# Kernel optimization log

Measured on AMD Instinct MI355X. Metric: run time of the kernel, lower is better.

## Reference

```python
import jax, jax.numpy as jnp
import numpy as np

FP4_AMAX = 6.0
FP8_AMAX = 448.0
E2M1_LUT = jnp.array([0.0, 0.5, 1.0, 1.5, 2.0, 3.0, 4.0, 6.0], dtype=jnp.float32)
# (threshold, code) pairs; applied in order, alternating <= and < comparisons
THRESHOLDS = [(5.0, 6), (3.5, 5), (2.5, 4), (1.75, 3), (1.25, 2), (0.75, 1), (0.25, 0)]


def _fp4_code(a):
    # a: abs-values, float32. Round-to-e2m1 magnitude code per the torch threshold table.
    code = jnp.full(a.shape, 7, dtype=jnp.int32)
    for i, (m, c) in enumerate(THRESHOLDS):
        mask = (a <= m) if i % 2 == 0 else (a < m)
        code = jnp.where(mask, c, code)
    return code


def simulate_nvfp4_quantize(w):
    # w: (out, in), in % 16 == 0. Returns fake-quantized weight, same shape/dtype.
    out_f, in_f = w.shape
    wb = w.reshape(out_f, in_f // 16, 16).astype(jnp.float32)
    gs = (FP4_AMAX * FP8_AMAX) / jnp.max(jnp.abs(wb))          # global fp32 scale
    s_decb = jnp.max(jnp.abs(wb), axis=-1) / FP4_AMAX           # per-16-block decode scale
    xs = jnp.clip(s_decb * gs, -FP8_AMAX, FP8_AMAX).astype(jnp.float8_e4m3fn)  # fp8 block scales
    xs_f = xs.astype(jnp.float32)
    s_encb = gs / jnp.clip(xs_f, 1e-12, None)                   # encode scale per block
    x_scaled = wb * s_encb[..., None]
    sign = jnp.where(jnp.signbit(x_scaled), -1.0, 1.0)
    mag = E2M1_LUT[_fp4_code(jnp.abs(x_scaled))]
    wq = sign * mag * (xs_f / gs)[..., None]                    # dequantize
    return wq.reshape(out_f, in_f).astype(w.dtype)


def setup_inputs() -> dict:
    key = jax.random.key(0)
    k1, k2, k3 = jax.random.split(key, 3)
    B, S, IN, OUT = 4, 2048, 4096, 4096
    x = jax.random.normal(k1, (B, S, IN), dtype=jnp.float32)
    weight = jax.random.normal(k2, (OUT, IN), dtype=jnp.float32) * 0.02
    bias = jax.random.normal(k3, (OUT,), dtype=jnp.float32) * 0.01
    return {"x": x, "weight": weight, "bias": bias}


def reference(x, weight, bias):
    # STE quantization: forward uses fake-quant weight
    weight_q = simulate_nvfp4_quantize(weight)
    # F.linear: x @ W^T + b
    return jnp.einsum("bsi,oi->bso", x, weight_q) + bias
```

## Files before the change

### kernel.cpp

```cpp
#include <hip/hip_runtime.h>
#include <hip/hip_bf16.h>
#include <stdint.h>

typedef __bf16 bf16_t;
typedef __bf16 bf16x8 __attribute__((ext_vector_type(8)));
typedef float  f32x4  __attribute__((ext_vector_type(4)));

#define BM 256
#define BN 256
#define BK 64
#define NTHREADS 512

__global__ void k_absmax(const float* __restrict__ w, unsigned int* __restrict__ out_bits, int n4) {
    int i = blockIdx.x * blockDim.x + threadIdx.x;
    int stride = gridDim.x * blockDim.x;
    const float4* w4 = (const float4*)w;
    float m = 0.0f;
    for (; i < n4; i += stride) {
        float4 v = w4[i];
        m = fmaxf(m, fmaxf(fmaxf(fabsf(v.x), fabsf(v.y)), fmaxf(fabsf(v.z), fabsf(v.w))));
    }
    #pragma unroll
    for (int off = 32; off; off >>= 1)
        m = fmaxf(m, __shfl_xor(m, off));
    if ((threadIdx.x & 63) == 0)
        atomicMax(out_bits, __float_as_uint(m));
}

__device__ __forceinline__ float e4m3_rne(float v) {
    if (v < 0.015625f) {
        return rintf(v * 512.0f) * (1.0f / 512.0f);
    }
    unsigned int u = __float_as_uint(v);
    unsigned int keep = u >> 20;
    unsigned int r = u & 0xFFFFFu;
    if (r > 0x80000u || (r == 0x80000u && (keep & 1u))) keep++;
    return __uint_as_float(keep << 20);
}

__global__ void k_quantize(const float* __restrict__ w, bf16_t* __restrict__ wq,
                           const unsigned int* __restrict__ maxbits, int nblk) {
    int t = blockIdx.x * blockDim.x + threadIdx.x;
    if (t >= nblk) return;
    float gmax = __uint_as_float(*maxbits);
    float gs = 2688.0f / gmax;
    const float4* w4 = (const float4*)w + (size_t)t * 4;
    float4 v0 = w4[0], v1 = w4[1], v2 = w4[2], v3 = w4[3];
    float vv[16];
    vv[0]=v0.x; vv[1]=v0.y; vv[2]=v0.z; vv[3]=v0.w;
    vv[4]=v1.x; vv[5]=v1.y; vv[6]=v1.z; vv[7]=v1.w;
    vv[8]=v2.x; vv[9]=v2.y; vv[10]=v2.z; vv[11]=v2.w;
    vv[12]=v3.x; vv[13]=v3.y; vv[14]=v3.z; vv[15]=v3.w;
    float bmax = 0.0f;
    #pragma unroll
    for (int j = 0; j < 16; ++j) bmax = fmaxf(bmax, fabsf(vv[j]));
    float s_decb = bmax / 6.0f;
    float xs_in  = fminf(s_decb * gs, 448.0f);
    float xs_f   = e4m3_rne(xs_in);
    float s_encb = gs / fmaxf(xs_f, 1e-12f);
    float dscale = xs_f / gs;
    bf16x8 o0, o1;
    #pragma unroll
    for (int j = 0; j < 16; ++j) {
        float xsc = vv[j] * s_encb;
        float a = fabsf(xsc);
        float mag = (a <= 0.25f) ? 0.0f
                  : (a <  0.75f) ? 0.5f
                  : (a <= 1.25f) ? 1.0f
                  : (a <  1.75f) ? 1.5f
                  : (a <= 2.5f ) ? 2.0f
                  : (a <  3.5f ) ? 3.0f
                  : (a <= 5.0f ) ? 4.0f : 6.0f;
        float sgn = __builtin_copysignf(1.0f, xsc);
        float val = (sgn * mag) * dscale;
        if (j < 8) o0[j] = (bf16_t)val; else o1[j - 8] = (bf16_t)val;
    }
    *(bf16x8*)(wq + (size_t)t * 16)     = o0;
    *(bf16x8*)(wq + (size_t)t * 16 + 8) = o1;
}

__global__ void k_cvt_x(const float* __restrict__ x, bf16_t* __restrict__ xb, long n8) {
    long i = blockIdx.x * (long)blockDim.x + threadIdx.x;
    long stride = (long)gridDim.x * blockDim.x;
    const float4* x4 = (const float4*)x;
    for (; i < n8; i += stride) {
        float4 a = x4[2 * i], b = x4[2 * i + 1];
        bf16x8 o;
        o[0] = (bf16_t)a.x; o[1] = (bf16_t)a.y; o[2] = (bf16_t)a.z; o[3] = (bf16_t)a.w;
        o[4] = (bf16_t)b.x; o[5] = (bf16_t)b.y; o[6] = (bf16_t)b.z; o[7] = (bf16_t)b.w;
        *(bf16x8*)(xb + i * 8) = o;
    }
}

__device__ __forceinline__ void BARRIER() {
    asm volatile("" ::: "memory");
    __builtin_amdgcn_s_barrier();
    asm volatile("" ::: "memory");
}

__device__ __forceinline__ void gload16(const bf16_t* g, bf16_t* l) {
    __builtin_amdgcn_global_load_lds(
        (const __attribute__((address_space(1))) unsigned int*)g,
        (__attribute__((address_space(3))) unsigned int*)l,
        16, 0, 0);
}

__global__ __launch_bounds__(NTHREADS, 2) void k_gemm(
        const bf16_t* __restrict__ A,
        const bf16_t* __restrict__ Bt,
        const float*  __restrict__ bias,
        float* __restrict__ C, int M, int N, int K) {
    __shared__ __align__(16) bf16_t sA[2][BM * BK];
    __shared__ __align__(16) bf16_t sB[2][BN * BK];

    int bid = blockIdx.x;
    int cpx = gridDim.x >> 3;
    int swz = (bid & 7) * cpx + (bid >> 3);
    int nbn = N / BN;
    int m0 = (swz / nbn) * BM, n0 = (swz % nbn) * BN;

    int tid  = threadIdx.x;
    int lane = tid & 63;
    int w    = tid >> 6;
    int wr   = w >> 2, wc = w & 3;
    int fr15 = lane & 15;
    int kg   = lane >> 4;

    int rowin = tid >> 3;
    int pg    = tid & 7;
    int gsw   = pg ^ (rowin & 7);
    int gstg[2], lstg[2];
    #pragma unroll
    for (int l = 0; l < 2; ++l) {
        gstg[l] = (l * 128 + rowin) * K + gsw * 8;
        lstg[l] = (l * 128 + rowin) * 64 + pg * 8;
    }
    int tq0 = tid >> 8;
    int rB  = (tid >> 3) & 31;
    int gbstg[2], lbstg[2];
    #pragma unroll
    for (int l = 0; l < 2; ++l) {
        int q = l * 2 + tq0;
        gbstg[l] = (q * 64 + rB) * K + gsw * 8;
        lbstg[l] = (q * 64 + rB) * 64 + pg * 8;
    }
    const bf16_t* Ab = A  + (size_t)m0 * K;
    const bf16_t* Bb = Bt + (size_t)n0 * K;

#define STGA(BUF, H, KT) do {                                                      \
        gload16(Ab + (H) * 64 * K + gstg[0] + (KT), &sA[BUF][(H) * 4096 + lstg[0]]); \
        gload16(Ab + (H) * 64 * K + gstg[1] + (KT), &sA[BUF][(H) * 4096 + lstg[1]]); \
    } while (0)
#define STGB(BUF, H, KT) do {                                                      \
        gload16(Bb + (H) * 32 * K + gbstg[0] + (KT), &sB[BUF][(H) * 2048 + lbstg[0]]); \
        gload16(Bb + (H) * 32 * K + gbstg[1] + (KT), &sB[BUF][(H) * 2048 + lbstg[1]]); \
    } while (0)

    int f01 = fr15 & 3, f2 = (fr15 >> 2) & 1;
    int pgr0 = 4 * (0 ^ f2) + (kg ^ f01);
    int pgr1 = 4 * (1 ^ f2) + (kg ^ f01);
    int baseA0 = (wr * 128 + fr15) * 64 + pgr0 * 8;
    int baseA1 = (wr * 128 + fr15) * 64 + pgr1 * 8;
    int baseB0 = (wc * 64  + fr15) * 64 + pgr0 * 8;
    int baseB1 = (wc * 64  + fr15) * 64 + pgr1 * 8;

    f32x4 acc[8][4] = {};
    bf16x8 afr[4][2];
    bf16x8 bfr[4][2];

    const int NT = K / BK;
    const int ITERS = NT / 2;

    STGB(0, 0, 0);  STGB(0, 1, 0);
    STGA(0, 0, 0);  STGA(0, 1, 0);
    STGB(1, 0, BK); STGB(1, 1, BK);
    STGA(1, 0, BK);
    asm volatile("s_waitcnt vmcnt(6)" ::: "memory");
    BARRIER();

#define RDA4(PA, MH) do {                                                          \
        _Pragma("unroll")                                                          \
        for (int m = 0; m < 4; ++m) {                                              \
            afr[m][0] = *(const bf16x8*)((PA) + baseA0 + ((MH) * 4 + m) * 1024);   \
            afr[m][1] = *(const bf16x8*)((PA) + baseA1 + ((MH) * 4 + m) * 1024);   \
        }                                                                          \
    } while (0)

#define RDB2(PB, NH) do {                                                          \
        _Pragma("unroll")                                                          \
        for (int j = 0; j < 2; ++j) {                                              \
            bfr[(NH)*2+j][0] = *(const bf16x8*)((PB) + baseB0 + ((NH)*2+j) * 1024);\
            bfr[(NH)*2+j][1] = *(const bf16x8*)((PB) + baseB1 + ((NH)*2+j) * 1024);\
        }                                                                          \
    } while (0)

#define MFQ(MH, NH) do {                                                                            \
        __builtin_amdgcn_s_setprio(1);                                                              \
        _Pragma("unroll")                                                                           \
        for (int n = 0; n < 2; ++n)                                                                 \
            _Pragma("unroll")                                                                       \
            for (int m = 0; m < 4; ++m)                                                             \
                acc[(MH)*4+m][(NH)*2+n] = __builtin_amdgcn_mfma_f32_16x16x32_bf16(                  \
                    afr[m][0], bfr[(NH)*2+n][0], acc[(MH)*4+m][(NH)*2+n], 0, 0, 0);                 \
        _Pragma("unroll")                                                                           \
        for (int n = 0; n < 2; ++n)                                                                 \
            _Pragma("unroll")                                                                       \
            for (int m = 0; m < 4; ++m)                                                             \
                acc[(MH)*4+m][(NH)*2+n] = __builtin_amdgcn_mfma_f32_16x16x32_bf16(                  \
                    afr[m][1], bfr[(NH)*2+n][1], acc[(MH)*4+m][(NH)*2+n], 0, 0, 0);                 \
        __builtin_amdgcn_s_setprio(0);                                                              \
    } while (0)

#define LGKM0() asm volatile("s_waitcnt lgkmcnt(0)" ::: "memory")

    for (int it = 0; it < ITERS; ++it) {
        const bool nl = (it + 1 < ITERS);
        const int ktB1 = (2 * it + 1) * BK;
        const int kt2  = (2 * it + 2) * BK;
        const int kt3  = (2 * it + 3) * BK;

        RDA4(sA[0], 0); RDB2(sB[0], 0);
        STGA(1, 1, ktB1);
        BARRIER(); LGKM0(); MFQ(0, 0); BARRIER();

        RDB2(sB[0], 1);
        if (nl) STGB(0, 0, kt2);
        BARRIER(); LGKM0(); MFQ(0, 1); BARRIER();

        RDA4(sA[0], 1);
        if (nl) STGB(0, 1, kt2);
        BARRIER(); LGKM0(); MFQ(1, 0); BARRIER();

        if (nl) STGA(0, 0, kt2);
        BARRIER(); MFQ(1, 1);
        if (nl) { asm volatile("s_waitcnt vmcnt(6)" ::: "memory"); }
        else    { asm volatile("s_waitcnt vmcnt(0)" ::: "memory"); }
        BARRIER();

        RDA4(sA[1], 0); RDB2(sB[1], 0);
        if (nl) STGA(0, 1, kt2);
        BARRIER(); LGKM0(); MFQ(0, 0); BARRIER();

        RDB2(sB[1], 1);
        if (nl) STGB(1, 0, kt3);
        BARRIER(); LGKM0(); MFQ(0, 1); BARRIER();

        RDA4(sA[1], 1);
        if (nl) STGB(1, 1, kt3);
        BARRIER(); LGKM0(); MFQ(1, 0); BARRIER();

        if (nl) STGA(1, 0, kt3);
        BARRIER(); MFQ(1, 1);
        if (nl) { asm volatile("s_waitcnt vmcnt(6)" ::: "memory"); }
        BARRIER();
    }
    asm volatile("s_waitcnt vmcnt(0)" ::: "memory");

    int crow = (lane >> 4) * 4;
    int ccol = lane & 15;
    float bv[4];
    #pragma unroll
    for (int j = 0; j < 4; ++j) bv[j] = bias[n0 + wc * 64 + j * 16 + ccol];
    #pragma unroll
    for (int i = 0; i < 8; ++i) {
        size_t mrow = (size_t)(m0 + wr * 128 + i * 16 + crow);
        #pragma unroll
        for (int j = 0; j < 4; ++j) {
            float* cp = C + mrow * N + (n0 + wc * 64 + j * 16 + ccol);
            #pragma unroll
            for (int r = 0; r < 4; ++r)
                cp[(size_t)r * N] = acc[i][j][r] + bv[j];
        }
    }
#undef STGA
#undef STGB
#undef RDA4
#undef RDB2
#undef MFQ
#undef LGKM0
}

extern "C" void kernel_launch(void* const* d_in, const int* in_sizes, int n_in,
                              void* d_out, int out_size, void* d_ws, size_t ws_size,
                              hipStream_t stream) {
    const float* x    = (const float*)d_in[0];
    const float* wgt  = (const float*)d_in[1];
    const float* bias = (const float*)d_in[2];
    float* out = (float*)d_out;

    const int N = in_sizes[2];
    const int K = in_sizes[1] / N;
    const int M = in_sizes[0] / K;

    unsigned int* maxbits = (unsigned int*)d_ws;
    bf16_t* wq = (bf16_t*)((char*)d_ws + 256);
    bf16_t* xb = (bf16_t*)((char*)d_ws + 256 + (size_t)N * K * sizeof(bf16_t));

    hipMemsetAsync(d_ws, 0, 256, stream);
    k_absmax<<<512, 256, 0, stream>>>(wgt, maxbits, N * K / 4);
    int nblk = N * K / 16;
    k_quantize<<<(nblk + 255) / 256, 256, 0, stream>>>(wgt, wq, maxbits, nblk);
    long n8 = (long)M * K / 8;
    k_cvt_x<<<2048, 256, 0, stream>>>(x, xb, n8);
    dim3 grid((M / BM) * (N / BN));
    k_gemm<<<grid, NTHREADS, 0, stream>>>(xb, wq, bias, out, M, N, K);
}
```

Baseline: 331.3 us.

## Software-pipeline LDS fragment reads ahead of MFMA quarters, drop explicit lgkm waits

Restructures the GEMM main loop so the LDS fragment loads for the next MFMA quarter are issued right after the current quarter's MFMAs, instead of load, barrier, wait, compute. This removes one barrier pair and the explicit lgkmcnt(0) stalls per quarter, so LDS reads overlap with matrix math. The first quarter's fragments are prefetched before the loop and again at the end of each iteration. The vmcnt wait placement is reworked to match. The risk is LDS race hazards when reads cross buffer phases, and higher register pressure.

```diff
diff --git a/kernel.cpp b/kernel.cpp
--- a/kernel.cpp
+++ b/kernel.cpp
@@ -180,18 +180,20 @@
 
 #define RDA4(PA, MH) do {                                                          \
         _Pragma("unroll")                                                          \
-        for (int m = 0; m < 4; ++m) {                                              \
+        for (int m = 0; m < 4; ++m)                                                \
             afr[m][0] = *(const bf16x8*)((PA) + baseA0 + ((MH) * 4 + m) * 1024);   \
+        _Pragma("unroll")                                                          \
+        for (int m = 0; m < 4; ++m)                                                \
             afr[m][1] = *(const bf16x8*)((PA) + baseA1 + ((MH) * 4 + m) * 1024);   \
-        }                                                                          \
     } while (0)
 
 #define RDB2(PB, NH) do {                                                          \
         _Pragma("unroll")                                                          \
-        for (int j = 0; j < 2; ++j) {                                              \
+        for (int j = 0; j < 2; ++j)                                                \
             bfr[(NH)*2+j][0] = *(const bf16x8*)((PB) + baseB0 + ((NH)*2+j) * 1024);\
+        _Pragma("unroll")                                                          \
+        for (int j = 0; j < 2; ++j)                                                \
             bfr[(NH)*2+j][1] = *(const bf16x8*)((PB) + baseB1 + ((NH)*2+j) * 1024);\
-        }                                                                          \
     } while (0)
 
 #define MFQ(MH, NH) do {                                                                            \
@@ -211,7 +213,7 @@
         __builtin_amdgcn_s_setprio(0);                                                              \
     } while (0)
 
-#define LGKM0() asm volatile("s_waitcnt lgkmcnt(0)" ::: "memory")
+    RDA4(sA[0], 0); RDB2(sB[0], 0);
 
     for (int it = 0; it < ITERS; ++it) {
         const bool nl = (it + 1 < ITERS);
@@ -219,39 +221,50 @@
         const int kt2  = (2 * it + 2) * BK;
         const int kt3  = (2 * it + 3) * BK;
 
-        RDA4(sA[0], 0); RDB2(sB[0], 0);
+        MFQ(0, 0);
+        RDB2(sB[0], 1);
         STGA(1, 1, ktB1);
-        BARRIER(); LGKM0(); MFQ(0, 0); BARRIER();
-
-        RDB2(sB[0], 1);
+        BARRIER();
+
+        MFQ(0, 1);
+        RDA4(sA[0], 1);
         if (nl) STGB(0, 0, kt2);
-        BARRIER(); LGKM0(); MFQ(0, 1); BARRIER();
-
-        RDA4(sA[0], 1);
+        BARRIER();
+
+        MFQ(1, 0);
         if (nl) STGB(0, 1, kt2);
-        BARRIER(); LGKM0(); MFQ(1, 0); BARRIER();
-
+        if (nl) { asm volatile("s_waitcnt vmcnt(6)" ::: "memory"); }
+        else    { asm volatile("s_waitcnt vmcnt(2)" ::: "memory"); }
+        BARRIER();
+
+        MFQ(1, 1);
         if (nl) STGA(0, 0, kt2);
-        BARRIER(); MFQ(1, 1);
         if (nl) { asm volatile("s_waitcnt vmcnt(6)" ::: "memory"); }
         else    { asm volatile("s_waitcnt vmcnt(0)" ::: "memory"); }
-        BARRIER();
-
         RDA4(sA[1], 0); RDB2(sB[1], 0);
+        BARRIER();
+
+        MFQ(0, 0);
+        RDB2(sB[1], 1);
         if (nl) STGA(0, 1, kt2);
-        BARRIER(); LGKM0(); MFQ(0, 0); BARRIER();
-
-        RDB2(sB[1], 1);
+        BARRIER();
+
+        MFQ(0, 1);
+        RDA4(sA[1], 1);
         if (nl) STGB(1, 0, kt3);
-        BARRIER(); LGKM0(); MFQ(0, 1); BARRIER();
-
-        RDA4(sA[1], 1);
+        BARRIER();
+
+        MFQ(1, 0);
         if (nl) STGB(1, 1, kt3);
-        BARRIER(); LGKM0(); MFQ(1, 0); BARRIER();
-
-        if (nl) STGA(1, 0, kt3);
-        BARRIER(); MFQ(1, 1);
-        if (nl) { asm volatile("s_waitcnt vmcnt(6)" ::: "memory"); }
+        asm volatile("s_waitcnt vmcnt(6)" ::: "memory");
+        BARRIER();
+
+        MFQ(1, 1);
+        if (nl) {
+            STGA(1, 0, kt3);
+            asm volatile("s_waitcnt vmcnt(6)" ::: "memory");
+            RDA4(sA[0], 0); RDB2(sB[0], 0);
+        }
         BARRIER();
     }
     asm volatile("s_waitcnt vmcnt(0)" ::: "memory");
@@ -277,7 +290,6 @@
 #undef RDA4
 #undef RDB2
 #undef MFQ
-#undef LGKM0
 }
 
 extern "C" void kernel_launch(void* const* d_in, const int* in_sizes, int n_in,
```

After: 361.9 us. 1.09x slower.
